# Kernel tuning notes

Measured on AMD Instinct MI355X. Metric: run time of the kernel, lower is better.

## Reference

```python
import jax, jax.numpy as jnp
import numpy as np

NUM_HEADS = 32
NUM_KV_HEADS = 8
HEAD_DIM = 128
ROPE_BASE = 10000.0


def _rope_tables(seq_len, head_dim, dtype):
    inv_freq = 1.0 / (ROPE_BASE ** (jnp.arange(0, head_dim, 2, dtype=jnp.float32) / head_dim))
    t = jnp.arange(seq_len, dtype=jnp.float32)
    freqs = jnp.einsum('i,j->ij', t, inv_freq)          # [S, D/2]
    emb = jnp.concatenate([freqs, freqs], axis=-1)      # [S, D]
    return jnp.cos(emb).astype(dtype), jnp.sin(emb).astype(dtype)


def _rotate_half(x):
    x1, x2 = jnp.split(x, 2, axis=-1)
    return jnp.concatenate([-x2, x1], axis=-1)


def _apply_rope(x, cos, sin):
    # x: [B, H, S, D]; cos/sin: [S, D] broadcast over batch and heads
    return x * cos[None, None, :, :] + _rotate_half(x) * sin[None, None, :, :]


def setup_inputs() -> dict:
    key = jax.random.key(0)
    k1, k2, k3, k4, k5 = jax.random.split(key, 5)
    B, S, H = 1, 2048, 4096
    scale = 0.02
    return {
        'hidden_states': jax.random.normal(k1, (B, S, H), dtype=jnp.float32),
        'Wq': jax.random.normal(k2, (4096, 4096), dtype=jnp.float32) * scale,
        'Wk': jax.random.normal(k3, (1024, 4096), dtype=jnp.float32) * scale,
        'Wv': jax.random.normal(k4, (1024, 4096), dtype=jnp.float32) * scale,
        'Wo': jax.random.normal(k5, (4096, 4096), dtype=jnp.float32) * scale,
    }


def reference(hidden_states, Wq, Wk, Wv, Wo):
    B, S, hidden = hidden_states.shape
    n_rep = NUM_HEADS // NUM_KV_HEADS

    # projections (torch Linear: y = x @ W.T)
    q = (hidden_states @ Wq.T).reshape(B, S, NUM_HEADS, HEAD_DIM).transpose(0, 2, 1, 3)
    k = (hidden_states @ Wk.T).reshape(B, S, NUM_KV_HEADS, HEAD_DIM).transpose(0, 2, 1, 3)
    v = (hidden_states @ Wv.T).reshape(B, S, NUM_KV_HEADS, HEAD_DIM).transpose(0, 2, 1, 3)

    # RoPE: init path with no past -> query/key position ids both arange(S)
    cos, sin = _rope_tables(S, HEAD_DIM, hidden_states.dtype)
    q = _apply_rope(q, cos, sin)
    k = _apply_rope(k, cos, sin)

    # repeat_kv: [B, Hkv, S, D] -> [B, H, S, D]
    k = jnp.repeat(k, n_rep, axis=1)
    v = jnp.repeat(v, n_rep, axis=1)

    # manual attention with causal mask
    scores = jnp.einsum('bhqd,bhkd->bhqk', q, k) / jnp.sqrt(jnp.float32(HEAD_DIM)).astype(q.dtype)
    causal = jnp.tril(jnp.ones((S, S), dtype=bool))
    scores = jnp.where(causal[None, None, :, :], scores, jnp.finfo(scores.dtype).min)
    probs = jax.nn.softmax(scores, axis=-1)

    out = jnp.einsum('bhqk,bhkd->bhqd', probs, v)        # [B, H, S, D]
    out = out.transpose(0, 2, 1, 3).reshape(B, S, hidden)
    return out @ Wo.T
```

## Files before the change

### kernel.cpp

```cpp
#include <hip/hip_runtime.h>
#include <hip/hip_bf16.h>

typedef __attribute__((ext_vector_type(4))) float f32x4;
typedef __attribute__((ext_vector_type(8))) short short8;
typedef __attribute__((ext_vector_type(4))) unsigned int u32x4;

__device__ __forceinline__ unsigned short f2bf(float f) {
  union { float f; unsigned int u; } v; v.f = f;
  unsigned int r = (v.u + 0x7fffu + ((v.u >> 16) & 1u)) >> 16;
  return (unsigned short)r;
}
__device__ __forceinline__ unsigned short f2bf_fast(float f) {
  __hip_bfloat16 h = __float2bfloat16(f);
  return __builtin_bit_cast(unsigned short, h);
}
__device__ __forceinline__ float bf2f(unsigned short h) {
  union { unsigned int u; float f; } v; v.u = ((unsigned int)h) << 16;
  return v.f;
}
__device__ __forceinline__ unsigned int cvt_pk_bf16(float lo, float hi) {
  unsigned int r;
  asm("v_cvt_pk_bf16_f32 %0, %1, %2" : "=v"(r) : "v"(lo), "v"(hi));
  return r;
}

__device__ __forceinline__ void gload_lds16(const void* g, void* l) {
  __builtin_amdgcn_global_load_lds((const __attribute__((address_space(1))) void*)g,
                                   (__attribute__((address_space(3))) void*)l,
                                   16, 0, 0);
}

template <int N>
__device__ __forceinline__ void vmwait() {
  asm volatile("s_waitcnt vmcnt(%0)" :: "n"(N) : "memory");
}

__global__ __launch_bounds__(256) void cvt_hid(const float* __restrict__ in,
                                               unsigned short* __restrict__ out,
                                               int n) {
  size_t stride = (size_t)gridDim.x * blockDim.x;
  for (size_t i = (size_t)blockIdx.x * blockDim.x + threadIdx.x; i * 4 < (size_t)n; i += stride) {
    float4 v = *(const float4*)(in + i * 4);
    ushort4 o;
    o.x = f2bf(v.x); o.y = f2bf(v.y); o.z = f2bf(v.z); o.w = f2bf(v.w);
    *(ushort4*)(out + i * 4) = o;
  }
}

template <int BM, int BN, bool BF16_OUT>
__global__ __launch_bounds__(256, 2) void gemm_f32b(
    const unsigned short* __restrict__ A,
    const float* __restrict__ B0, const float* __restrict__ B1,
    const float* __restrict__ B2, int b1, int b2,
    void* __restrict__ Cout, int M, int N, int K) {
  constexpr int BK = 64;
  constexpr int MFRAG = BM / 32;
  constexpr int NFRAG = BN / 32;
  constexpr int ASH = BM * BK;
  constexpr int BSH = BN * BK;
  constexpr int BUF = ASH + BSH;
  constexpr int ALOADS = BM / 32;
  constexpr int BLOADS = BN / 32;
  __shared__ unsigned short lds[2 * BUF];

  const int tid = threadIdx.x;
  const int wave = tid >> 6, lane = tid & 63;
  const int l15 = lane & 15, l4 = lane >> 4;
  const int row0 = blockIdx.y * BM, col0 = blockIdx.x * BN;
  const int mrow0 = (wave >> 1) * (BM / 2);
  const int ncol0 = (wave & 1) * (BN / 2);
  const int NT = K >> 6;
  const int srow = tid >> 3;
  const int spsw = (tid & 7) ^ (srow & 7);

  f32x4 zv = {0.f, 0.f, 0.f, 0.f};
  f32x4 acc[MFRAG][NFRAG];
#pragma unroll
  for (int m = 0; m < MFRAG; ++m)
#pragma unroll
    for (int n = 0; n < NFRAG; ++n) acc[m][n] = zv;

  float4 br[2 * BLOADS];

  auto stageA = [&](int t) {
    unsigned short* buf = &lds[(t & 1) * BUF];
    const int k0 = t * BK;
#pragma unroll
    for (int i = 0; i < ALOADS; ++i)
      gload_lds16(A + (size_t)(row0 + i * 32 + srow) * K + k0 + spsw * 8,
                  buf + i * 2048 + tid * 8);
  };
  auto loadB = [&](int t) {
    const int k0 = t * BK;
#pragma unroll
    for (int i = 0; i < BLOADS; ++i) {
      int grow = col0 + i * 32;
      const float* src; int rrow;
      if (grow < b1)      { src = B0; rrow = grow; }
      else if (grow < b2) { src = B1; rrow = grow - b1; }
      else                { src = B2; rrow = grow - b2; }
      const float* p = src + (size_t)(rrow + srow) * K + k0 + spsw * 8;
      br[2 * i]     = *(const float4*)p;
      br[2 * i + 1] = *(const float4*)(p + 4);
    }
  };
  auto writeB = [&](int t) {
    unsigned short* buf = &lds[(t & 1) * BUF];
#pragma unroll
    for (int i = 0; i < BLOADS; ++i) {
      u32x4 w;
      w[0] = cvt_pk_bf16(br[2 * i].x, br[2 * i].y);
      w[1] = cvt_pk_bf16(br[2 * i].z, br[2 * i].w);
      w[2] = cvt_pk_bf16(br[2 * i + 1].x, br[2 * i + 1].y);
      w[3] = cvt_pk_bf16(br[2 * i + 1].z, br[2 * i + 1].w);
      *(u32x4*)&buf[ASH + i * 2048 + tid * 8] = w;
    }
  };

  stageA(0);
  loadB(0);
  vmwait<0>();
  writeB(0);

  for (int t = 0; t < NT; ++t) {
    asm volatile("s_waitcnt lgkmcnt(0)" ::: "memory");
    __builtin_amdgcn_sched_barrier(0);
    __builtin_amdgcn_s_barrier();
    __builtin_amdgcn_sched_barrier(0);
    const bool hn = (t + 1 < NT);
    if (hn) { stageA(t + 1); loadB(t + 1); }

    const unsigned short* Ab = &lds[(t & 1) * BUF];
    const unsigned short* Bb = Ab + ASH;
#pragma unroll
    for (int h = 0; h < 2; ++h) {
      short8 afr[MFRAG], bfr[NFRAG];
#pragma unroll
      for (int m = 0; m < MFRAG; ++m) {
        int row = mrow0 + m * 16 + l15;
        afr[m] = *(const short8*)&Ab[row * 64 + (((h * 4 + l4) ^ (l15 & 7)) * 8)];
      }
#pragma unroll
      for (int n = 0; n < NFRAG; ++n) {
        int row = ncol0 + n * 16 + l15;
        bfr[n] = *(const short8*)&Bb[row * 64 + (((h * 4 + l4) ^ (l15 & 7)) * 8)];
      }
      __builtin_amdgcn_s_setprio(1);
#pragma unroll
      for (int m = 0; m < MFRAG; ++m)
#pragma unroll
        for (int n = 0; n < NFRAG; ++n)
          acc[m][n] = __builtin_amdgcn_mfma_f32_16x16x32_bf16(afr[m], bfr[n], acc[m][n], 0, 0, 0);
      __builtin_amdgcn_s_setprio(0);
    }

    if (hn) {
      vmwait<0>();
      __builtin_amdgcn_sched_barrier(0);
      writeB(t + 1);
    }
  }

#pragma unroll
  for (int m = 0; m < MFRAG; ++m)
#pragma unroll
    for (int n = 0; n < NFRAG; ++n)
#pragma unroll
      for (int j = 0; j < 4; ++j) {
        int r = row0 + mrow0 + m * 16 + l4 * 4 + j;
        int cc = col0 + ncol0 + n * 16 + l15;
        if constexpr (BF16_OUT)
          ((unsigned short*)Cout)[(size_t)r * N + cc] = f2bf(acc[m][n][j]);
        else
          ((float*)Cout)[(size_t)r * N + cc] = acc[m][n][j];
      }
}

__global__ __launch_bounds__(256) void rope_k(unsigned short* __restrict__ QKV) {
  int idx = blockIdx.x * blockDim.x + threadIdx.x;
  if (idx >= 2048 * 40 * 64) return;
  int j = idx & 63;
  int rest = idx >> 6;
  int slot = rest % 40;
  int s = rest / 40;
  int doff = (slot < 32) ? slot * 128 : 4096 + (slot - 32) * 128;
  unsigned short* p = QKV + (size_t)s * 6144 + doff;
  float inv = exp2f((float)j * -0.20762050593046015f);
  float ang = (float)s * inv;
  float sn, cs;
  sincosf(ang, &sn, &cs);
  float x1 = bf2f(p[j]), x2 = bf2f(p[j + 64]);
  p[j]      = f2bf(x1 * cs - x2 * sn);
  p[j + 64] = f2bf(x2 * cs + x1 * sn);
}

__global__ __launch_bounds__(512, 4) void attn_k(
    const unsigned short* __restrict__ QKV,
    unsigned short* __restrict__ O) {
  __shared__ unsigned short Ks[2][64 * 128];
  __shared__ unsigned short Vs[2][64 * 128];

  const int tid = threadIdx.x;
  const int wave = tid >> 6, lane = tid & 63;
  const int l15 = lane & 15, l4 = lane >> 4;

  const int bid = blockIdx.x;
  const int qt16 = bid & 15;
  const int h = (bid >> 4) & 31;
  const int qt = (h < 16) ? (15 - qt16) : qt16;
  const int hkv = h >> 2;
  const int q0 = qt * 128;
  const int qrow = q0 + wave * 16 + l15;
  const float C2 = 0.12751744219938793f;

  const unsigned short* Qp = QKV + h * 128;
  const unsigned short* Kp = QKV + 4096 + hkv * 128;
  const unsigned short* Vp = QKV + 5120 + hkv * 128;

  const int vpr = tid >> 4;
  const int vd8 = tid & 15;
  const int vg8 = vpr >> 2, vjj = 2 * (vpr & 3);
  const int vn = vd8 >> 1, vch = (vd8 & 1) * 8;

  short8 qf[4];
#pragma unroll
  for (int kc = 0; kc < 4; ++kc)
    qf[kc] = *(const short8*)(Qp + (size_t)qrow * 6144 + kc * 32 + l4 * 8);

  f32x4 zv = {0.f, 0.f, 0.f, 0.f};
  f32x4 oacc[8];
#pragma unroll
  for (int n = 0; n < 8; ++n) oacc[n] = zv;
  float mrow = -3.0e38f, lrow = 0.f;

  auto stageK = [&](int kvn, int b) {
#pragma unroll
    for (int i = 0; i < 2; ++i) {
      int c = wave * 2 + i;
      int row = c * 4 + l4;
      int colel = (l15 * 8) ^ ((row & 7) << 3);
      gload_lds16(Kp + (size_t)(kvn + row) * 6144 + colel, &Ks[b][c * 512]);
    }
  };
  auto loadV = [&](int kvn, short8& va, short8& vb) {
    va = *(const short8*)(Vp + (size_t)(kvn + 2 * vpr) * 6144 + vd8 * 8);
    vb = *(const short8*)(Vp + (size_t)(kvn + 2 * vpr + 1) * 6144 + vd8 * 8);
  };
  auto writeV = [&](int b, const short8& va, const short8& vb) {
#pragma unroll
    for (int i = 0; i < 8; ++i) {
      int c = vch + i;
      unsigned int pack = (unsigned int)(unsigned short)va[i] |
                          ((unsigned int)(unsigned short)vb[i] << 16);
      *(unsigned int*)&Vs[b][vg8 * 1024 + vn * 128 + ((c ^ vn) & 15) * 8 + vjj] = pack;
    }
  };

  {
    short8 va, vb;
    stageK(0, 0);
    loadV(0, va, vb);
    writeV(0, va, vb);
  }
  __syncthreads();

  const int nt = 2 * qt + 2;
  for (int t = 0; t < nt; ++t) {
    const int cur = t & 1, nxt = cur ^ 1;
    const int kv0 = t * 64;
    const bool has_next = (t + 1 < nt);
    short8 va, vb;
    if (has_next) {
      stageK(kv0 + 64, nxt);
      loadV(kv0 + 64, va, vb);
    }

    f32x4 sacc[4];
#pragma unroll
    for (int cb = 0; cb < 4; ++cb) sacc[cb] = zv;
    __builtin_amdgcn_s_setprio(1);
#pragma unroll
    for (int cb = 0; cb < 4; ++cb) {
      int row = cb * 16 + l15;
      int sw = (row & 7) << 3;
#pragma unroll
      for (int kc = 0; kc < 4; ++kc) {
        short8 kf = *(const short8*)&Ks[cur][row * 128 + ((kc * 32 + l4 * 8) ^ sw)];
        sacc[cb] = __builtin_amdgcn_mfma_f32_16x16x32_bf16(kf, qf[kc], sacc[cb], 0, 0, 0);
      }
    }
    __builtin_amdgcn_s_setprio(0);

    if (kv0 + 63 > q0 + wave * 16) {
#pragma unroll
      for (int cb = 0; cb < 4; ++cb)
#pragma unroll
        for (int j = 0; j < 4; ++j) {
          int kvpos = kv0 + cb * 16 + l4 * 4 + j;
          if (kvpos > qrow) sacc[cb][j] = -3.0e38f;
        }
    }

    float pm = sacc[0][0];
#pragma unroll
    for (int cb = 0; cb < 4; ++cb)
#pragma unroll
      for (int j = 0; j < 4; ++j) pm = fmaxf(pm, sacc[cb][j]);
    pm = fmaxf(pm, __shfl_xor(pm, 16, 64));
    pm = fmaxf(pm, __shfl_xor(pm, 32, 64));

    if (__any(pm > mrow + 64.0f)) {
      float mn = fmaxf(mrow, pm);
      float rs = exp2f((mrow - mn) * C2);
      mrow = mn;
      lrow *= rs;
      float rs0 = __shfl(rs, 4 * l4 + 0, 64);
      float rs1 = __shfl(rs, 4 * l4 + 1, 64);
      float rs2 = __shfl(rs, 4 * l4 + 2, 64);
      float rs3 = __shfl(rs, 4 * l4 + 3, 64);
#pragma unroll
      for (int n = 0; n < 8; ++n) {
        oacc[n][0] *= rs0; oacc[n][1] *= rs1;
        oacc[n][2] *= rs2; oacc[n][3] *= rs3;
      }
    }

    unsigned int pack[8];
    float psum = 0.f;
#pragma unroll
    for (int cb = 0; cb < 4; ++cb) {
      float p0 = exp2f((sacc[cb][0] - mrow) * C2);
      float p1 = exp2f((sacc[cb][1] - mrow) * C2);
      float p2 = exp2f((sacc[cb][2] - mrow) * C2);
      float p3 = exp2f((sacc[cb][3] - mrow) * C2);
      psum += (p0 + p1) + (p2 + p3);
      pack[cb * 2 + 0] = cvt_pk_bf16(p0, p1);
      pack[cb * 2 + 1] = cvt_pk_bf16(p2, p3);
    }
    lrow += psum;

#pragma unroll
    for (int ks = 0; ks < 2; ++ks) {
      u32x4 pw;
#pragma unroll
      for (int w = 0; w < 4; ++w) {
        int sl = l15 + 16 * ((2 * l4 + (w >> 1)) & 3);
        int v0 = __shfl((int)pack[4 * ks + (w & 1)], sl, 64);
        int v1 = __shfl((int)pack[4 * ks + 2 + (w & 1)], sl, 64);
        pw[w] = (lane < 32) ? (unsigned int)v0 : (unsigned int)v1;
      }
      short8 pf = __builtin_bit_cast(short8, pw);
      __builtin_amdgcn_s_setprio(1);
#pragma unroll
      for (int n = 0; n < 8; ++n) {
        short8 vf = *(const short8*)&Vs[cur][(ks * 4 + l4) * 1024 + n * 128 + ((l15 ^ n) & 15) * 8];
        oacc[n] = __builtin_amdgcn_mfma_f32_16x16x32_bf16(pf, vf, oacc[n], 0, 0, 0);
      }
      __builtin_amdgcn_s_setprio(0);
    }

    if (has_next) writeV(nxt, va, vb);
    __syncthreads();
  }

  lrow += __shfl_xor(lrow, 16, 64);
  lrow += __shfl_xor(lrow, 32, 64);
  float linv = 1.0f / lrow;
  float li0 = __shfl(linv, 4 * l4 + 0, 64);
  float li1 = __shfl(linv, 4 * l4 + 1, 64);
  float li2 = __shfl(linv, 4 * l4 + 2, 64);
  float li3 = __shfl(linv, 4 * l4 + 3, 64);
#pragma unroll
  for (int n = 0; n < 8; ++n) {
    int r = q0 + wave * 16 + l4 * 4;
    size_t base = (size_t)r * 4096 + h * 128 + n * 16 + l15;
    O[base]          = f2bf_fast(oacc[n][0] * li0);
    O[base + 4096]   = f2bf_fast(oacc[n][1] * li1);
    O[base + 8192]   = f2bf_fast(oacc[n][2] * li2);
    O[base + 12288]  = f2bf_fast(oacc[n][3] * li3);
  }
}

extern "C" void kernel_launch(void* const* d_in, const int* in_sizes, int n_in,
                              void* d_out, int out_size, void* d_ws, size_t ws_size,
                              hipStream_t stream) {
  const float* hid = (const float*)d_in[0];
  const float* Wq  = (const float*)d_in[1];
  const float* Wk  = (const float*)d_in[2];
  const float* Wv  = (const float*)d_in[3];
  const float* Wo  = (const float*)d_in[4];

  char* ws = (char*)d_ws;
  size_t off = 0;
  unsigned short* hid_b = (unsigned short*)(ws + off); off += (size_t)2048 * 4096 * 2;
  unsigned short* QKV   = (unsigned short*)(ws + off); off += (size_t)2048 * 6144 * 2;
  unsigned short* Ob    = (unsigned short*)(ws + off); off += (size_t)2048 * 4096 * 2;

  cvt_hid<<<2048, 256, 0, stream>>>(hid, hid_b, 2048 * 4096);

  gemm_f32b<128, 192, true><<<dim3(32, 16), 256, 0, stream>>>(
      hid_b, Wq, Wk, Wv, 4096, 5120, (void*)QKV, 2048, 6144, 4096);

  rope_k<<<20480, 256, 0, stream>>>(QKV);

  attn_k<<<512, 512, 0, stream>>>(QKV, Ob);

  gemm_f32b<128, 128, false><<<dim3(32, 16), 256, 0, stream>>>(
      Ob, Wo, Wo, Wo, 4096, 4096, d_out, 2048, 4096, 4096);
}
```

Before: 318.8 us.

## Prefetch fp32 B tiles two iterations ahead with double register buffers

The GEMM main loop now keeps two register buffers for the fp32 B operand. Global loads for tile t+2 are issued while tile t is computed, and the A tile moves to LDS one step ahead. Partial vmcnt waits replace full drains, so B load latency gets a whole extra iteration to hide. The cost is more VGPRs under the 2-blocks-per-SM launch bound, which may cause spills or lower occupancy, plus a hand-unrolled loop that assumes NT is even and at least 2.

```diff
diff --git a/kernel.cpp b/kernel.cpp
--- a/kernel.cpp
+++ b/kernel.cpp
@@ -33,6 +33,9 @@
 template <int N>
 __device__ __forceinline__ void vmwait() {
   asm volatile("s_waitcnt vmcnt(%0)" :: "n"(N) : "memory");
+}
+__device__ __forceinline__ void lgkm0() {
+  asm volatile("s_waitcnt lgkmcnt(0)" ::: "memory");
 }
 
 __global__ __launch_bounds__(256) void cvt_hid(const float* __restrict__ in,
@@ -46,6 +49,33 @@
     *(ushort4*)(out + i * 4) = o;
   }
 }
+
+#define LOADB(T, BR)                                                          \
+  {                                                                           \
+    const int k0 = (T) * BK;                                                  \
+    _Pragma("unroll") for (int i = 0; i < BLOADS; ++i) {                      \
+      int grow = col0 + i * 32;                                               \
+      const float* src; int rrow;                                             \
+      if (grow < b1)      { src = B0; rrow = grow; }                          \
+      else if (grow < b2) { src = B1; rrow = grow - b1; }                     \
+      else                { src = B2; rrow = grow - b2; }                     \
+      const float* p = src + (size_t)(rrow + srow) * K + k0 + spsw * 8;       \
+      BR[2 * i]     = *(const float4*)p;                                      \
+      BR[2 * i + 1] = *(const float4*)(p + 4);                                \
+    }                                                                         \
+  }
+#define WRITEB(T, BR)                                                         \
+  {                                                                           \
+    unsigned short* buf = &lds[((T) & 1) * BUF];                              \
+    _Pragma("unroll") for (int i = 0; i < BLOADS; ++i) {                      \
+      u32x4 w;                                                                \
+      w[0] = cvt_pk_bf16(BR[2 * i].x, BR[2 * i].y);                           \
+      w[1] = cvt_pk_bf16(BR[2 * i].z, BR[2 * i].w);                           \
+      w[2] = cvt_pk_bf16(BR[2 * i + 1].x, BR[2 * i + 1].y);                   \
+      w[3] = cvt_pk_bf16(BR[2 * i + 1].z, BR[2 * i + 1].w);                   \
+      *(u32x4*)&buf[ASH + i * 2048 + tid * 8] = w;                            \
+    }                                                                         \
+  }
 
 template <int BM, int BN, bool BF16_OUT>
 __global__ __launch_bounds__(256, 2) void gemm_f32b(
@@ -61,6 +91,9 @@
   constexpr int BUF = ASH + BSH;
   constexpr int ALOADS = BM / 32;
   constexpr int BLOADS = BN / 32;
+  constexpr int NB = 2 * BLOADS;
+  constexpr int TOPW = NB;
+  constexpr int ENDW = ALOADS + NB;
   __shared__ unsigned short lds[2 * BUF];
 
   const int tid = threadIdx.x;
@@ -80,7 +113,7 @@
 #pragma unroll
     for (int n = 0; n < NFRAG; ++n) acc[m][n] = zv;
 
-  float4 br[2 * BLOADS];
+  float4 brA[NB], brB[NB];
 
   auto stageA = [&](int t) {
     unsigned short* buf = &lds[(t & 1) * BUF];
@@ -90,46 +123,7 @@
       gload_lds16(A + (size_t)(row0 + i * 32 + srow) * K + k0 + spsw * 8,
                   buf + i * 2048 + tid * 8);
   };
-  auto loadB = [&](int t) {
-    const int k0 = t * BK;
-#pragma unroll
-    for (int i = 0; i < BLOADS; ++i) {
-      int grow = col0 + i * 32;
-      const float* src; int rrow;
-      if (grow < b1)      { src = B0; rrow = grow; }
-      else if (grow < b2) { src = B1; rrow = grow - b1; }
-      else                { src = B2; rrow = grow - b2; }
-      const float* p = src + (size_t)(rrow + srow) * K + k0 + spsw * 8;
-      br[2 * i]     = *(const float4*)p;
-      br[2 * i + 1] = *(const float4*)(p + 4);
-    }
-  };
-  auto writeB = [&](int t) {
-    unsigned short* buf = &lds[(t & 1) * BUF];
-#pragma unroll
-    for (int i = 0; i < BLOADS; ++i) {
-      u32x4 w;
-      w[0] = cvt_pk_bf16(br[2 * i].x, br[2 * i].y);
-      w[1] = cvt_pk_bf16(br[2 * i].z, br[2 * i].w);
-      w[2] = cvt_pk_bf16(br[2 * i + 1].x, br[2 * i + 1].y);
-      w[3] = cvt_pk_bf16(br[2 * i + 1].z, br[2 * i + 1].w);
-      *(u32x4*)&buf[ASH + i * 2048 + tid * 8] = w;
-    }
-  };
-
-  stageA(0);
-  loadB(0);
-  vmwait<0>();
-  writeB(0);
-
-  for (int t = 0; t < NT; ++t) {
-    asm volatile("s_waitcnt lgkmcnt(0)" ::: "memory");
-    __builtin_amdgcn_sched_barrier(0);
-    __builtin_amdgcn_s_barrier();
-    __builtin_amdgcn_sched_barrier(0);
-    const bool hn = (t + 1 < NT);
-    if (hn) { stageA(t + 1); loadB(t + 1); }
-
+  auto compute = [&](int t) {
     const unsigned short* Ab = &lds[(t & 1) * BUF];
     const unsigned short* Bb = Ab + ASH;
 #pragma unroll
@@ -153,13 +147,53 @@
           acc[m][n] = __builtin_amdgcn_mfma_f32_16x16x32_bf16(afr[m], bfr[n], acc[m][n], 0, 0, 0);
       __builtin_amdgcn_s_setprio(0);
     }
-
-    if (hn) {
-      vmwait<0>();
-      __builtin_amdgcn_sched_barrier(0);
-      writeB(t + 1);
-    }
-  }
+  };
+
+  LOADB(0, brA);
+  vmwait<0>();
+  WRITEB(0, brA);
+  stageA(0);
+  LOADB(1, brB);
+
+  for (int t = 0; t < NT - 2; t += 2) {
+    vmwait<TOPW>();
+    lgkm0();
+    __builtin_amdgcn_sched_barrier(0);
+    __builtin_amdgcn_s_barrier();
+    __builtin_amdgcn_sched_barrier(0);
+    stageA(t + 1);
+    LOADB(t + 2, brA);
+    compute(t);
+    vmwait<ENDW>();
+    __builtin_amdgcn_sched_barrier(0);
+    WRITEB(t + 1, brB);
+    vmwait<TOPW>();
+    lgkm0();
+    __builtin_amdgcn_sched_barrier(0);
+    __builtin_amdgcn_s_barrier();
+    __builtin_amdgcn_sched_barrier(0);
+    stageA(t + 2);
+    LOADB(t + 3, brB);
+    compute(t + 1);
+    vmwait<ENDW>();
+    __builtin_amdgcn_sched_barrier(0);
+    WRITEB(t + 2, brA);
+  }
+
+  vmwait<0>();
+  lgkm0();
+  __builtin_amdgcn_sched_barrier(0);
+  __builtin_amdgcn_s_barrier();
+  __builtin_amdgcn_sched_barrier(0);
+  stageA(NT - 1);
+  compute(NT - 2);
+  WRITEB(NT - 1, brB);
+  vmwait<0>();
+  lgkm0();
+  __builtin_amdgcn_sched_barrier(0);
+  __builtin_amdgcn_s_barrier();
+  __builtin_amdgcn_sched_barrier(0);
+  compute(NT - 1);
 
 #pragma unroll
   for (int m = 0; m < MFRAG; ++m)
```

Measured after the change: 469.4 us. 1.47x slower.

## Pre-convert QKV weights to bf16 and use all-bf16 async-LDS GEMM

Applied to the files above, without the earlier changes.

The single conversion kernel now turns hidden states and the Wq/Wk/Wv weights into one contiguous bf16 buffer. The QKV projection then runs a new GEMM that streams both operands as bf16 through global-to-LDS direct loads, replacing the kernel that read fp32 weights and converted them inside the GEMM. This moves the per-tile weight conversion out of the inner loop and halves B-operand traffic during the GEMM. In exchange, an extra pass reads the fp32 weights and writes bf16 copies every call, which adds roughly 96MB of traffic.

```diff
diff --git a/kernel.cpp b/kernel.cpp
--- a/kernel.cpp
+++ b/kernel.cpp
@@ -35,16 +35,119 @@
   asm volatile("s_waitcnt vmcnt(%0)" :: "n"(N) : "memory");
 }
 
-__global__ __launch_bounds__(256) void cvt_hid(const float* __restrict__ in,
-                                               unsigned short* __restrict__ out,
-                                               int n) {
+__global__ __launch_bounds__(256) void cvt_all(
+    const float* __restrict__ hid, const float* __restrict__ wq,
+    const float* __restrict__ wk, const float* __restrict__ wv,
+    unsigned short* __restrict__ out) {
+  const size_t E0 = 8388608, E1 = 25165824, E2 = 29360128, E3 = 33554432;
   size_t stride = (size_t)gridDim.x * blockDim.x;
-  for (size_t i = (size_t)blockIdx.x * blockDim.x + threadIdx.x; i * 4 < (size_t)n; i += stride) {
-    float4 v = *(const float4*)(in + i * 4);
+  for (size_t i = (size_t)blockIdx.x * blockDim.x + threadIdx.x; i * 4 < E3; i += stride) {
+    size_t i4 = i * 4;
+    const float* src; size_t rel;
+    if (i4 < E0)      { src = hid; rel = i4; }
+    else if (i4 < E1) { src = wq;  rel = i4 - E0; }
+    else if (i4 < E2) { src = wk;  rel = i4 - E1; }
+    else              { src = wv;  rel = i4 - E2; }
+    float4 v = *(const float4*)(src + rel);
     ushort4 o;
     o.x = f2bf(v.x); o.y = f2bf(v.y); o.z = f2bf(v.z); o.w = f2bf(v.w);
-    *(ushort4*)(out + i * 4) = o;
+    *(ushort4*)(out + i4) = o;
   }
+}
+
+template <int BM, int BN, bool BF16_OUT>
+__global__ __launch_bounds__(256, 2) void gemm_p2(
+    const unsigned short* __restrict__ A,
+    const unsigned short* __restrict__ B,
+    void* __restrict__ Cout, int M, int N, int K) {
+  constexpr int BK = 64;
+  constexpr int MFRAG = BM / 32;
+  constexpr int NFRAG = BN / 32;
+  constexpr int ASH = BM * BK;
+  constexpr int BSH = BN * BK;
+  constexpr int BUF = ASH + BSH;
+  constexpr int ALOADS = BM / 32;
+  constexpr int BLOADS = BN / 32;
+  __shared__ unsigned short lds[2 * BUF];
+
+  const int tid = threadIdx.x;
+  const int wave = tid >> 6, lane = tid & 63;
+  const int l15 = lane & 15, l4 = lane >> 4;
+  const int row0 = blockIdx.y * BM, col0 = blockIdx.x * BN;
+  const int mrow0 = (wave >> 1) * (BM / 2);
+  const int ncol0 = (wave & 1) * (BN / 2);
+  const int NT = K >> 6;
+  const int srow = tid >> 3;
+  const int scol = ((tid & 7) ^ (srow & 7)) * 8;
+
+  f32x4 zv = {0.f, 0.f, 0.f, 0.f};
+  f32x4 acc[MFRAG][NFRAG];
+#pragma unroll
+  for (int m = 0; m < MFRAG; ++m)
+#pragma unroll
+    for (int n = 0; n < NFRAG; ++n) acc[m][n] = zv;
+
+  auto stage = [&](int t) {
+    unsigned short* buf = &lds[(t & 1) * BUF];
+    const int k0 = t * BK;
+#pragma unroll
+    for (int i = 0; i < ALOADS; ++i)
+      gload_lds16(A + (size_t)(row0 + i * 32 + srow) * K + k0 + scol,
+                  buf + i * 2048 + tid * 8);
+#pragma unroll
+    for (int i = 0; i < BLOADS; ++i)
+      gload_lds16(B + (size_t)(col0 + i * 32 + srow) * K + k0 + scol,
+                  buf + ASH + i * 2048 + tid * 8);
+  };
+
+  stage(0);
+
+  for (int t = 0; t < NT; ++t) {
+    vmwait<0>();
+    __builtin_amdgcn_sched_barrier(0);
+    __builtin_amdgcn_s_barrier();
+    __builtin_amdgcn_sched_barrier(0);
+    if (t + 1 < NT) stage(t + 1);
+
+    const unsigned short* Ab = &lds[(t & 1) * BUF];
+    const unsigned short* Bb = Ab + ASH;
+#pragma unroll
+    for (int h = 0; h < 2; ++h) {
+      short8 afr[MFRAG], bfr[NFRAG];
+#pragma unroll
+      for (int m = 0; m < MFRAG; ++m) {
+        int row = mrow0 + m * 16 + l15;
+        afr[m] = *(const short8*)&Ab[row * 64 + (((h * 4 + l4) ^ (l15 & 7)) * 8)];
+      }
+#pragma unroll
+      for (int n = 0; n < NFRAG; ++n) {
+        int row = ncol0 + n * 16 + l15;
+        bfr[n] = *(const short8*)&Bb[row * 64 + (((h * 4 + l4) ^ (l15 & 7)) * 8)];
+      }
+      __builtin_amdgcn_s_setprio(1);
+#pragma unroll
+      for (int m = 0; m < MFRAG; ++m)
+#pragma unroll
+        for (int n = 0; n < NFRAG; ++n)
+          acc[m][n] = __builtin_amdgcn_mfma_f32_16x16x32_bf16(afr[m], bfr[n], acc[m][n], 0, 0, 0);
+      __builtin_amdgcn_s_setprio(0);
+    }
+    __builtin_amdgcn_sched_barrier(0);
+  }
+
+#pragma unroll
+  for (int m = 0; m < MFRAG; ++m)
+#pragma unroll
+    for (int n = 0; n < NFRAG; ++n)
+#pragma unroll
+      for (int j = 0; j < 4; ++j) {
+        int r = row0 + mrow0 + m * 16 + l4 * 4 + j;
+        int cc = col0 + ncol0 + n * 16 + l15;
+        if constexpr (BF16_OUT)
+          ((unsigned short*)Cout)[(size_t)r * N + cc] = f2bf(acc[m][n][j]);
+        else
+          ((float*)Cout)[(size_t)r * N + cc] = acc[m][n][j];
+      }
 }
 
 template <int BM, int BN, bool BF16_OUT>
@@ -393,13 +496,16 @@
   char* ws = (char*)d_ws;
   size_t off = 0;
   unsigned short* hid_b = (unsigned short*)(ws + off); off += (size_t)2048 * 4096 * 2;
+  unsigned short* Wq_b  = (unsigned short*)(ws + off); off += (size_t)4096 * 4096 * 2;
+  unsigned short* Wk_b  = (unsigned short*)(ws + off); off += (size_t)1024 * 4096 * 2;
+  unsigned short* Wv_b  = (unsigned short*)(ws + off); off += (size_t)1024 * 4096 * 2;
   unsigned short* QKV   = (unsigned short*)(ws + off); off += (size_t)2048 * 6144 * 2;
   unsigned short* Ob    = (unsigned short*)(ws + off); off += (size_t)2048 * 4096 * 2;
-
-  cvt_hid<<<2048, 256, 0, stream>>>(hid, hid_b, 2048 * 4096);
-
-  gemm_f32b<128, 192, true><<<dim3(32, 16), 256, 0, stream>>>(
-      hid_b, Wq, Wk, Wv, 4096, 5120, (void*)QKV, 2048, 6144, 4096);
+  (void)Wk_b; (void)Wv_b;
+
+  cvt_all<<<4096, 256, 0, stream>>>(hid, Wq, Wk, Wv, hid_b);
+
+  gemm_p2<128, 192, true><<<dim3(32, 16), 256, 0, stream>>>(hid_b, Wq_b, (void*)QKV, 2048, 6144, 4096);
 
   rope_k<<<20480, 256, 0, stream>>>(QKV);
 
```

Result: slower. 328.5 us (+3.0%).
